# Kernel tuning notes

Hardware: AMD Instinct MI355X
Metric: run time of the kernel (lower is better)

## Reference

```python
import jax, jax.numpy as jnp
import numpy as np

NUM_CLASSES = 80
C_OUT = 81
SCORE_THR = 0.02
IOU_THR = 0.45
TOPK = 1000
IMG_MAX = 320.0
STRIDES = [16, 32, 64, 107, 160, 320]
MIN_SIZES = [48, 100, 150, 202, 253, 304]
MAX_SIZES = [100, 150, 202, 253, 304, 320]
FEAT = [20, 10, 5, 3, 2, 1]
MAX_RATIO = float(abs(np.log(0.016)))


def _base_anchors(level):
    base = float(MIN_SIZES[level])
    scales = np.array([1.0, np.sqrt(MAX_SIZES[level] / MIN_SIZES[level])])
    ratios = np.array([1.0, 0.5, 2.0, 1.0 / 3.0, 3.0])
    h_ratios = np.sqrt(ratios)
    w_ratios = 1.0 / h_ratios
    # scale_major=False: scales vary along rows
    ws = (base * scales[:, None] * w_ratios[None, :]).reshape(-1)
    hs = (base * scales[:, None] * h_ratios[None, :]).reshape(-1)
    c = STRIDES[level] / 2.0
    ba = np.stack([c - 0.5 * ws, c - 0.5 * hs, c + 0.5 * ws, c + 0.5 * hs], -1)
    return ba[[0, 5, 1, 2, 3, 4]]  # index_select reorder, 6 anchors/loc


def _priors(level):
    ba = _base_anchors(level)
    f, s = FEAT[level], STRIDES[level]
    sx = np.arange(f, dtype=np.float64) * s
    xx = np.tile(sx, f)
    yy = np.repeat(sx, f)
    shifts = np.stack([xx, yy, xx, yy], -1)  # [f*f,4]
    return (ba[None, :, :] + shifts[:, None, :]).reshape(-1, 4).astype(np.float32)


PRIORS = [jnp.asarray(_priors(i)) for i in range(6)]


def delta2bbox(priors, deltas):
    stds = jnp.array([0.1, 0.1, 0.2, 0.2], dtype=deltas.dtype)
    d = deltas * stds
    pxy = (priors[:, :2] + priors[:, 2:]) * 0.5
    pwh = priors[:, 2:] - priors[:, :2]
    dwh = jnp.clip(d[:, 2:], -MAX_RATIO, MAX_RATIO)
    gxy = pxy + pwh * d[:, :2]
    gwh = pwh * jnp.exp(dwh)
    boxes = jnp.concatenate([gxy - 0.5 * gwh, gxy + 0.5 * gwh], -1)
    return jnp.clip(boxes, 0.0, IMG_MAX)


def _nms_keep(boxes, valid, iou_thr):
    # greedy NMS over score-sorted boxes; returns bool keep mask
    K = boxes.shape[0]
    area = (boxes[:, 2] - boxes[:, 0]) * (boxes[:, 3] - boxes[:, 1])
    lt = jnp.maximum(boxes[:, None, :2], boxes[None, :, :2])
    rb = jnp.minimum(boxes[:, None, 2:], boxes[None, :, 2:])
    wh = jnp.clip(rb - lt, 0.0)
    inter = wh[..., 0] * wh[..., 1]
    iou = inter / (area[:, None] + area[None, :] - inter)
    ar = jnp.arange(K)

    def body(i, alive):
        sup = (iou[i] > iou_thr) & (ar > i) & alive[i]
        return alive & ~sup

    return jax.lax.fori_loop(0, K, body, valid)


def _single_image(cls_list, bb_list):
    boxes_l, scores_l, labels_l, valid_l = [], [], [], []
    for cls, bb, priors in zip(cls_list, bb_list, PRIORS):
        probs = jax.nn.softmax(cls.transpose(1, 2, 0).reshape(-1, C_OUT), axis=-1)[:, :NUM_CLASSES]
        flat = probs.reshape(-1)  # [N*80]
        k = min(TOPK, flat.shape[0])
        masked = jnp.where(flat > SCORE_THR, flat, -1.0)
        vals, idx = jax.lax.top_k(masked, k)
        valid = vals > SCORE_THR
        a_idx = idx // NUM_CLASSES
        lbl = idx % NUM_CLASSES
        deltas = bb.transpose(1, 2, 0).reshape(-1, 4)[a_idx]
        boxes = delta2bbox(priors[a_idx], deltas)
        boxes_l.append(boxes)
        scores_l.append(jnp.where(valid, vals, 0.0))
        labels_l.append(lbl)
        valid_l.append(valid)
    boxes = jnp.concatenate(boxes_l, 0)   # [K,4]
    scores = jnp.concatenate(scores_l, 0)
    labels = jnp.concatenate(labels_l, 0)
    valid = jnp.concatenate(valid_l, 0)

    # batched (class-aware) NMS via per-class coordinate offsets
    max_coord = boxes.max()
    offsets = labels.astype(boxes.dtype) * (max_coord + 1.0)
    boxes_nms = boxes + offsets[:, None]
    order = jnp.argsort(-jnp.where(valid, scores, -jnp.inf))
    boxes_s = boxes[order]
    scores_s = scores[order]
    labels_s = labels[order]
    valid_s = valid[order]
    keep = jax.lax.stop_gradient(
        _nms_keep(jax.lax.stop_gradient(boxes_nms[order]), valid_s, IOU_THR))
    dets = jnp.concatenate([boxes_s, scores_s[:, None]], -1) * keep[:, None].astype(boxes.dtype)
    return dets, labels_s, keep


def setup_inputs() -> dict:
    key = jax.random.key(0)
    ks = jax.random.split(key, 12)
    B = 4
    inp = {}
    for i, f in enumerate(FEAT):
        inp[f"cls{i}"] = jax.random.normal(ks[i], (B, 486, f, f), dtype=jnp.float32)
        inp[f"bb{i}"] = jax.random.normal(ks[6 + i], (B, 24, f, f), dtype=jnp.float32)
    return inp


def reference(cls0, cls1, cls2, cls3, cls4, cls5, bb0, bb1, bb2, bb3, bb4, bb5):
    def one(c0, c1, c2, c3, c4, c5, b0, b1, b2, b3, b4, b5):
        return _single_image([c0, c1, c2, c3, c4, c5], [b0, b1, b2, b3, b4, b5])
    dets, labels, keep = jax.vmap(one)(cls0, cls1, cls2, cls3, cls4, cls5,
                                       bb0, bb1, bb2, bb3, bb4, bb5)
    return dets, labels, keep
```

## Files before the change

kernel.cpp:

```cpp
#include <hip/hip_runtime.h>
#include <stdint.h>

#define NB 4
#define KTOT 5480
#define PER_IMG 258720
#define SCORE_THR 0.02f
#define IOU_THR 0.45f
#define REL_BASE 0x3CA3D70Bu
#define JCH 10
#define JSZ 548
#define ICH 11
#define NMSCAP 512
#define HBINS 256
#define HPART 42

__constant__ int cFEAT[6]    = {20,10,5,3,2,1};
__constant__ int cSTRIDE[6]  = {16,32,64,107,160,320};
__constant__ int cMIN[6]     = {48,100,150,202,253,304};
__constant__ int cMAX[6]     = {100,150,202,253,304,320};
__constant__ int cNFLAT[6]   = {192000,48000,12000,4320,1920,480};
__constant__ int cFLATOFF[6] = {0,192000,240000,252000,256320,258240};
__constant__ int cKSEL[6]    = {1000,1000,1000,1000,1000,480};
__constant__ int cKOFF[6]    = {0,1000,2000,3000,4000,5000};
__constant__ double cRATIO[6] = {1.0,1.0,0.5,2.0,1.0/3.0,3.0};
__constant__ int eTLEV[24] = {0,0,0,0,0,0,0,0,0,0,0,0,0,0,0,0, 1,1,1,1, 2,3,4,5};
__constant__ int eTCHK[24] = {0,1,2,3,4,5,6,7,8,9,10,11,12,13,14,15, 0,1,2,3, 0,0,0,0};
__constant__ int eNCH[6]   = {16,4,1,1,1,1};
__constant__ int hL0[6]    = {0,42,54,60,66,72};
__constant__ int hLN[6]    = {42,12,6,6,6,6};

__device__ __forceinline__ unsigned long long mk_key(unsigned kb, int lev, unsigned idx) {
  return ((unsigned long long)kb << 21) |
         (unsigned long long)(0x1FFFFFu ^ (((unsigned)lev << 18) | idx));
}

__device__ __forceinline__ unsigned long long shfl64(unsigned long long x, int src) {
  int lo = __shfl((int)(unsigned)(x & 0xffffffffull), src);
  int hi = __shfl((int)(unsigned)(x >> 32), src);
  return ((unsigned long long)(unsigned)hi << 32) | (unsigned)lo;
}

__global__ __launch_bounds__(256) void k_softmax(
    const float* __restrict__ c0, const float* __restrict__ c1,
    const float* __restrict__ c2, const float* __restrict__ c3,
    const float* __restrict__ c4, const float* __restrict__ c5,
    float* __restrict__ scores, unsigned* __restrict__ bhist,
    unsigned* __restrict__ obmax_u, unsigned* __restrict__ ctrl)
{
  int t = blockIdx.x;
  int tid = threadIdx.x;
  if (t == 0) {
    if (tid < 4) obmax_u[tid] = 0u;
    if (tid >= 64 && tid < 256) ctrl[tid - 64] = 0u;
  }
  int b = t / 78, rem = t % 78;
  int lev, a, cb;
  if (rem < 42)      { lev = 0; a = rem / 7;         cb = (rem % 7) * 64; }
  else if (rem < 54) { lev = 1; a = (rem - 42) >> 1; cb = ((rem - 42) & 1) * 64; }
  else               { lev = 2 + (rem - 54) / 6; a = (rem - 54) % 6; cb = 0; }
  const float* cls = (lev==0)?c0:(lev==1)?c1:(lev==2)?c2:(lev==3)?c3:(lev==4)?c4:c5;
  int f = cFEAT[lev], ff = f * f;
  int ncell = ff - cb; if (ncell > 64) ncell = 64;

  __shared__ float tile[81 * 64];
  __shared__ unsigned hcnt[HBINS];
  if (tid < HBINS) hcnt[tid] = 0;
  const float* base = cls + (size_t)(b * 486 + a * 81) * ff + cb;
  for (int t2 = tid; t2 < 81 * 64; t2 += 256) {
    int c = t2 >> 6, cell = t2 & 63;
    if (cell < ncell)
      tile[(c << 6) | (cell ^ (c & 63))] = base[c * ff + cell];
  }
  __syncthreads();

  int lane = tid & 63, w = tid >> 6;
  for (int cell = w; cell < ncell; cell += 4) {
    float v1 = tile[(lane << 6) | (cell ^ lane)];
    float v2 = (lane <= 16) ? tile[((lane + 64) << 6) | (cell ^ lane)]
                            : __uint_as_float(0xff800000u);
    float mx = fmaxf(v1, v2);
    #pragma unroll
    for (int m = 32; m; m >>= 1) mx = fmaxf(mx, __shfl_xor(mx, m));
    float e1 = expf(v1 - mx);
    float e2 = (lane <= 16) ? expf(v2 - mx) : 0.f;
    float sm = e1 + e2;
    #pragma unroll
    for (int m = 32; m; m >>= 1) sm += __shfl_xor(sm, m);
    int row = (cb + cell) * 6 + a;
    float* out = scores + (size_t)b * PER_IMG + cFLATOFF[lev] + row * 80;
    float p1 = e1 / sm;
    out[lane] = (p1 > SCORE_THR) ? p1 : -1.f;
    if (p1 > SCORE_THR)
      atomicAdd(&hcnt[(__float_as_uint(p1) - REL_BASE) >> 18], 1u);
    if (lane < 16) {
      float p2 = e2 / sm;
      out[lane + 64] = (p2 > SCORE_THR) ? p2 : -1.f;
      if (p2 > SCORE_THR)
        atomicAdd(&hcnt[(__float_as_uint(p2) - REL_BASE) >> 18], 1u);
    }
  }
  __syncthreads();
  int task = b * 6 + lev;
  int j = rem - hL0[lev];
  if (tid < HBINS)
    bhist[((size_t)task * HBINS + tid) * HPART + j] = hcnt[tid];
}

__global__ __launch_bounds__(256) void k_emit(
    const float* __restrict__ scores, const unsigned* __restrict__ bhist,
    unsigned* __restrict__ ctrl, unsigned long long* __restrict__ selkeys,
    unsigned long long* __restrict__ eqg)
{
  int b = blockIdx.x / 24, ent = blockIdx.x % 24;
  int lev = eTLEV[ent], chk = eTCHK[ent];
  int task = b * 6 + lev;
  int n = cNFLAT[lev];
  int tid = threadIdx.x;
  const float* s = scores + (size_t)b * PER_IMG + cFLATOFF[lev];
  unsigned long long* out = selkeys + (size_t)b * KTOT + cKOFF[lev];

  if (lev == 5) {
    for (int i = tid; i < n; i += 256) {
      float v = s[i];
      unsigned kb = (v > SCORE_THR) ? __float_as_uint(v) : 0u;
      out[i] = mk_key(kb, lev, (unsigned)i);
    }
    return;
  }

  unsigned k = (unsigned)cKSEL[lev];
  __shared__ unsigned long long wbuf[1024];
  __shared__ unsigned long long ebuf[4096];
  __shared__ unsigned sc[256];
  __shared__ unsigned wcnt, ecnt, sbw, sbe, sh_mode, sh_b1;

  {
    const unsigned* hb = bhist + ((size_t)task * HBINS + tid) * HPART;
    int np = hLN[lev];
    unsigned cnt = 0;
    for (int j = 0; j < np; ++j) cnt += hb[j];
    sc[tid] = cnt;
    __syncthreads();
    for (int off = 1; off < 256; off <<= 1) {
      unsigned cur = sc[tid];
      unsigned add = (tid + off < 256) ? sc[tid + off] : 0u;
      __syncthreads();
      sc[tid] = cur + add;
      __syncthreads();
    }
    unsigned c = sc[0];
    if (tid == 0 && c < k) sh_mode = 1u;
    if (c >= k) {
      unsigned above = (tid == 255) ? 0u : sc[tid + 1];
      if (above < k && above + cnt >= k) { sh_mode = 0u; sh_b1 = (unsigned)tid; }
    }
    if (tid == 0) { wcnt = 0; ecnt = 0; }
    __syncthreads();
  }
  unsigned mode = sh_mode;

  int csz = n / eNCH[lev];
  int start = chk * csz;
  const float4* s4 = (const float4*)(s + start);
  int n4 = csz >> 2;

  if (mode == 0u) {
    unsigned b1 = sh_b1;
    unsigned base_lo = REL_BASE + (b1 << 18);
    unsigned base_hi = base_lo + (1u << 18);
    #pragma unroll 4
    for (int i0 = tid; i0 < n4; i0 += 256) {
      float4 vv = s4[i0];
      #pragma unroll
      for (int e2 = 0; e2 < 4; ++e2) {
        float v = (e2==0)?vv.x:(e2==1)?vv.y:(e2==2)?vv.z:vv.w;
        if (v > SCORE_THR) {
          unsigned kb = __float_as_uint(v);
          unsigned idx = (unsigned)(start + i0 * 4 + e2);
          if (kb >= base_hi) {
            unsigned p = atomicAdd(&wcnt, 1u);
            if (p < 1024u) wbuf[p] = mk_key(kb, lev, idx);
          } else if (kb >= base_lo) {
            unsigned p = atomicAdd(&ecnt, 1u);
            if (p < 4096u) ebuf[p] = mk_key(kb, lev, idx);
          }
        }
      }
    }
  } else {
    #pragma unroll 4
    for (int i0 = tid; i0 < n4; i0 += 256) {
      float4 vv = s4[i0];
      #pragma unroll
      for (int e2 = 0; e2 < 4; ++e2) {
        float v = (e2==0)?vv.x:(e2==1)?vv.y:(e2==2)?vv.z:vv.w;
        if (v > SCORE_THR) {
          unsigned p = atomicAdd(&wcnt, 1u);
          if (p < 1024u) wbuf[p] = mk_key(__float_as_uint(v), lev,
                                          (unsigned)(start + i0 * 4 + e2));
        }
      }
    }
  }
  __syncthreads();
  if (tid == 0) {
    sbw = atomicAdd(&ctrl[task * 8 + 2], wcnt);
    sbe = atomicAdd(&ctrl[task * 8 + 3], ecnt);
  }
  __syncthreads();
  unsigned nw = (wcnt < 1024u) ? wcnt : 1024u;
  unsigned ne = (ecnt < 4096u) ? ecnt : 4096u;
  unsigned bw = sbw, be = sbe;
  for (unsigned t = tid; t < nw; t += 256) out[bw + t] = wbuf[t];
  for (unsigned t = tid; t < ne; t += 256) {
    unsigned g = be + t;
    if (g < 4096u) eqg[(size_t)task * 4096 + g] = ebuf[t];
  }
}

__global__ __launch_bounds__(1024) void k_finalize(
    const float* __restrict__ scores, const unsigned* __restrict__ bhist,
    const unsigned* __restrict__ ctrl, unsigned long long* __restrict__ selkeys,
    const unsigned long long* __restrict__ eqg)
{
  int task = blockIdx.x;
  int b = task / 6, lev = task % 6;
  if (lev == 5) return;
  int tid = threadIdx.x;
  unsigned k = (unsigned)cKSEL[lev];
  int n = cNFLAT[lev];
  const float* s = scores + (size_t)b * PER_IMG + cFLATOFF[lev];
  unsigned long long* out = selkeys + (size_t)b * KTOT + cKOFF[lev];
  unsigned levtag = (unsigned)lev << 18;

  __shared__ unsigned long long eqb[4096];
  __shared__ unsigned sc[1024];
  __shared__ unsigned sh_cnt, sh_eq, sh_byte, sh_r;

  unsigned hval = 0;
  if (tid < HBINS) {
    const unsigned* hb = bhist + ((size_t)task * HBINS + tid) * HPART;
    int np = hLN[lev];
    for (int j = 0; j < np; ++j) hval += hb[j];
  }
  sc[tid] = (tid < HBINS) ? hval : 0u;
  __syncthreads();
  for (int off = 128; off >= 1; off >>= 1) {
    if (tid < off) sc[tid] += sc[tid + off];
    __syncthreads();
  }
  unsigned c = sc[0];
  __syncthreads();
  unsigned mode = (c >= k) ? 0u : 1u;
  bool done = false;

  if (mode == 0u) {
    unsigned cnt = ctrl[task * 8 + 2];
    unsigned e = ctrl[task * 8 + 3];
    unsigned need = k - cnt;
    if (e <= 4096u) {
      const unsigned long long* eq = eqg + (size_t)task * 4096;
      if (e == need) {
        for (unsigned t = tid; t < need; t += 1024) out[cnt + t] = eq[t];
      } else {
        unsigned P = 1; while (P < e) P <<= 1;
        for (unsigned t = tid; t < P; t += 1024) eqb[t] = (t < e) ? eq[t] : 0ull;
        __syncthreads();
        for (unsigned sz = 2; sz <= P; sz <<= 1)
          for (unsigned st = sz >> 1; st; st >>= 1) {
            for (unsigned w = tid; w < P / 2; w += 1024) {
              unsigned i = ((w & ~(st - 1)) << 1) | (w & (st - 1));
              unsigned l = i | st;
              bool up = ((i & sz) == 0);
              unsigned long long A = eqb[i], B = eqb[l];
              if ((A < B) == up) { eqb[i] = B; eqb[l] = A; }
            }
            __syncthreads();
          }
        for (unsigned t = tid; t < need; t += 1024) out[cnt + t] = eqb[t];
      }
      done = true;
    }
  } else {
    unsigned c2 = ctrl[task * 8 + 2];
    unsigned need = k - c2;
    unsigned base = 0;
    for (int start = 0; start < n && base < need; start += 1024) {
      int i = start + tid;
      unsigned pred = (i < n && !(s[i] > SCORE_THR)) ? 1u : 0u;
      sc[tid] = pred;
      __syncthreads();
      for (int off = 1; off < 1024; off <<= 1) {
        unsigned add = (tid >= off) ? sc[tid - off] : 0u;
        unsigned v = sc[tid];
        __syncthreads();
        sc[tid] = v + add;
        __syncthreads();
      }
      unsigned incl = sc[tid];
      unsigned total = sc[1023];
      unsigned excl = incl - pred;
      if (pred && (base + excl) < need)
        out[c2 + base + excl] =
            (unsigned long long)(0x1FFFFFu ^ (levtag | (unsigned)i));
      __syncthreads();
      base += total;
    }
    done = true;
  }

  if (!done) {
    unsigned* hist = sc;
    unsigned* equ = (unsigned*)eqb;
    unsigned prefix = 0, r = k;
    for (int pass = 3; pass >= 0; --pass) {
      int shift = pass * 8;
      for (int i = tid; i < 256; i += 1024) hist[i] = 0;
      __syncthreads();
      for (int i = tid; i < n; i += 1024) {
        float v = s[i];
        unsigned kb = (v > SCORE_THR) ? __float_as_uint(v) : 0u;
        bool match = (pass == 3) || (((kb ^ prefix) >> (shift + 8)) == 0u);
        if (match) atomicAdd(&hist[(kb >> shift) & 255u], 1u);
      }
      __syncthreads();
      if (tid == 0) {
        unsigned cum = 0, byte = 0, rr = r;
        for (int bb = 255; bb >= 0; --bb) {
          unsigned hh = hist[bb];
          if (cum + hh >= r) { byte = (unsigned)bb; rr = r - cum; break; }
          cum += hh;
        }
        sh_byte = byte; sh_r = rr;
      }
      __syncthreads();
      prefix |= (sh_byte << shift);
      r = sh_r;
      __syncthreads();
    }
    unsigned Kstar = prefix;
    if (tid == 0) { sh_cnt = 0; sh_eq = 0; }
    __syncthreads();
    for (int i = tid; i < n; i += 1024) {
      float v = s[i];
      unsigned kb = (v > SCORE_THR) ? __float_as_uint(v) : 0u;
      if (kb > Kstar) {
        unsigned slot = atomicAdd(&sh_cnt, 1u);
        out[slot] = mk_key(kb, lev, (unsigned)i);
      } else if (kb == Kstar) {
        unsigned es = atomicAdd(&sh_eq, 1u);
        if (es < 4096u) equ[es] = (unsigned)i;
      }
    }
    __syncthreads();
    unsigned m = sh_cnt;
    unsigned e2 = (sh_eq < 4096u) ? sh_eq : 4096u;
    unsigned need2 = k - m;
    if (e2 > need2) {
      unsigned P = 1; while (P < e2) P <<= 1;
      for (unsigned t = tid; t < P; t += 1024) if (t >= e2) equ[t] = 0xFFFFFFFFu;
      __syncthreads();
      for (unsigned sz = 2; sz <= P; sz <<= 1)
        for (unsigned st = sz >> 1; st; st >>= 1) {
          for (unsigned w = tid; w < P / 2; w += 1024) {
            unsigned i = ((w & ~(st - 1)) << 1) | (w & (st - 1));
            unsigned l = i | st;
            bool up = ((i & sz) == 0);
            unsigned A = equ[i], B = equ[l];
            if ((A > B) == up) { equ[i] = B; equ[l] = A; }
          }
          __syncthreads();
        }
    }
    __syncthreads();
    for (unsigned t = tid; t < need2; t += 1024)
      out[m + t] = ((unsigned long long)Kstar << 21) |
                   (unsigned long long)(0x1FFFFFu ^ (levtag | equ[t]));
  }
}

__global__ __launch_bounds__(512) void k_rank(
    const unsigned long long* __restrict__ selkeys, unsigned* __restrict__ rank_part)
{
  int blk = blockIdx.x;
  int jc = blk % JCH;
  int rest = blk / JCH;
  int ic = rest % ICH, b = rest / ICH;
  int tid = threadIdx.x;
  __shared__ __align__(16) unsigned long long sk[JSZ];
  const unsigned long long* keys = selkeys + (size_t)b * KTOT;
  for (int j = tid; j < JSZ; j += 512) sk[j] = keys[jc * JSZ + j];
  int i = ic * 512 + tid;
  unsigned long long mk = (i < KTOT) ? keys[i] : 0ull;
  __syncthreads();
  unsigned r = 0;
  const ulonglong2* sk2 = (const ulonglong2*)sk;
  #pragma unroll 8
  for (int j = 0; j < JSZ / 2; ++j) {
    ulonglong2 kk = sk2[j];
    r += (kk.x > mk) ? 1u : 0u;
    r += (kk.y > mk) ? 1u : 0u;
  }
  if (i < KTOT) rank_part[((size_t)jc * NB + b) * KTOT + i] = r;
}

__global__ __launch_bounds__(512) void k_decode(
    const unsigned long long* __restrict__ selkeys, const unsigned* __restrict__ rank_part,
    const float* __restrict__ g0, const float* __restrict__ g1,
    const float* __restrict__ g2, const float* __restrict__ g3,
    const float* __restrict__ g4, const float* __restrict__ g5,
    float* __restrict__ boxes, float* __restrict__ oscore,
    unsigned char* __restrict__ lab8, unsigned* __restrict__ obmax_u,
    float* __restrict__ outp)
{
  int b = blockIdx.x / ICH, ic = blockIdx.x % ICH;
  int tid = threadIdx.x;
  int i = ic * 512 + tid;
  __shared__ double ba[6][6][4];
  if (tid < 36) {
    int lev = tid / 6, a = tid % 6;
    double base = (double)cMIN[lev];
    double scl = (a == 1) ? sqrt((double)cMAX[lev] / (double)cMIN[lev]) : 1.0;
    double hr = sqrt(cRATIO[a]);
    double wr = 1.0 / hr;
    double wsz = base * scl * wr;
    double hsz = base * scl * hr;
    double cc = (double)cSTRIDE[lev] / 2.0;
    ba[lev][a][0] = cc - 0.5 * wsz;
    ba[lev][a][1] = cc - 0.5 * hsz;
    ba[lev][a][2] = cc + 0.5 * wsz;
    ba[lev][a][3] = cc + 0.5 * hsz;
  }
  __syncthreads();

  float lmax = 0.f;
  if (i < KTOT) {
    unsigned long long mk = selkeys[(size_t)b * KTOT + i];
    unsigned r = 0;
    #pragma unroll
    for (int jc = 0; jc < JCH; ++jc)
      r += rank_part[((size_t)jc * NB + b) * KTOT + i];
    unsigned tag = 0x1FFFFFu ^ (unsigned)(mk & 0x1FFFFFull);
    int lev = tag >> 18;
    int fi = tag & 0x3FFFF;
    unsigned vb2 = (unsigned)(mk >> 21);
    int valid = (vb2 != 0u);
    float score = valid ? __uint_as_float(vb2) : 0.f;
    int label = fi % 80;
    int arow = fi / 80;
    int a = arow % 6, cell = arow / 6;
    int f = cFEAT[lev], ff = f * f;
    int x = cell % f, y = cell / f;
    const float* gb = (lev==0)?g0:(lev==1)?g1:(lev==2)?g2:(lev==3)?g3:(lev==4)?g4:g5;
    const float* pb = gb + (size_t)(b * 24 + a * 4) * ff + y * f + x;
    float d0 = pb[0] * 0.1f, d1 = pb[ff] * 0.1f;
    float d2 = pb[2 * ff] * 0.2f, d3 = pb[3 * ff] * 0.2f;
    const float MR = (float)4.135166556742356;
    d2 = fminf(fmaxf(d2, -MR), MR);
    d3 = fminf(fmaxf(d3, -MR), MR);
    double shx = (double)(x * cSTRIDE[lev]);
    double shy = (double)(y * cSTRIDE[lev]);
    float p0 = (float)(ba[lev][a][0] + shx);
    float p1 = (float)(ba[lev][a][1] + shy);
    float p2 = (float)(ba[lev][a][2] + shx);
    float p3 = (float)(ba[lev][a][3] + shy);
    float pxc = (p0 + p2) * 0.5f, pyc = (p1 + p3) * 0.5f;
    float pw = p2 - p0, ph = p3 - p1;
    float gx = pxc + pw * d0, gy = pyc + ph * d1;
    float gw = pw * expf(d2), gh = ph * expf(d3);
    float x1 = gx - 0.5f * gw, y1 = gy - 0.5f * gh;
    float x2 = gx + 0.5f * gw, y2 = gy + 0.5f * gh;
    x1 = fminf(fmaxf(x1, 0.f), 320.f);
    y1 = fminf(fmaxf(y1, 0.f), 320.f);
    x2 = fminf(fmaxf(x2, 0.f), 320.f);
    y2 = fminf(fmaxf(y2, 0.f), 320.f);
    size_t o = (size_t)b * KTOT + (size_t)r;
    boxes[o * 4 + 0] = x1; boxes[o * 4 + 1] = y1;
    boxes[o * 4 + 2] = x2; boxes[o * 4 + 3] = y2;
    oscore[o] = score;
    lab8[o] = valid ? (unsigned char)label : (unsigned char)0xFF;
    outp[(size_t)NB * KTOT * 5 + o] = (float)label;
    if (!valid) {
      float* det = outp + o * 5;
      det[0] = 0.f; det[1] = 0.f; det[2] = 0.f; det[3] = 0.f; det[4] = 0.f;
      outp[(size_t)NB * KTOT * 6 + o] = 0.f;
    }
    lmax = fmaxf(fmaxf(x1, y1), fmaxf(x2, y2));
  }
  #pragma unroll
  for (int m = 32; m; m >>= 1) lmax = fmaxf(lmax, __shfl_xor(lmax, m));
  if ((tid & 63) == 0) atomicMax(&obmax_u[b], __float_as_uint(lmax));
}

__global__ __launch_bounds__(256) void k_nms(
    const float* __restrict__ boxes, const float* __restrict__ oscore,
    const unsigned char* __restrict__ lab8, const unsigned* __restrict__ obmax_u,
    float* __restrict__ out)
{
  int blk = blockIdx.x;
  int b = blk / 80, cls = blk % 80;
  int tid = threadIdx.x;
  int lane = tid & 63, w = tid >> 6;

  __shared__ unsigned short list[NMSCAP];
  __shared__ float ox1[NMSCAP], oy1[NMSCAP], ox2[NMSCAP], oy2[NMSCAP];
  __shared__ float oar[NMSCAP], osc[NMSCAP];
  __shared__ float rx1[NMSCAP], ry1[NMSCAP], rx2[NMSCAP], ry2[NMSCAP];
  __shared__ unsigned long long mask[NMSCAP][8];
  __shared__ unsigned ccnt[24], cbase[24];
  __shared__ int sh_n;
  __shared__ unsigned long long alive_s[8];

  float ofs = (float)cls * (__uint_as_float(obmax_u[b]) + 1.0f);
  const unsigned* lb32 = (const unsigned*)(lab8 + (size_t)b * KTOT);

  unsigned long long balA[6][4];
  #pragma unroll
  for (int ci = 0; ci < 6; ++ci) {
    int chunk = w + ci * 4;
    unsigned v = 0xFFFFFFFFu;
    if (chunk < 22) {
      int u = chunk * 64 + lane;
      if (u < KTOT / 4) v = lb32[u];
    }
    unsigned long long m0 = __ballot(((v      ) & 0xFFu) == (unsigned)cls);
    unsigned long long m1 = __ballot(((v >>  8) & 0xFFu) == (unsigned)cls);
    unsigned long long m2 = __ballot(((v >> 16) & 0xFFu) == (unsigned)cls);
    unsigned long long m3 = __ballot(((v >> 24) & 0xFFu) == (unsigned)cls);
    balA[ci][0] = m0; balA[ci][1] = m1; balA[ci][2] = m2; balA[ci][3] = m3;
    if (chunk < 22 && lane == 0)
      ccnt[chunk] = (unsigned)(__popcll(m0) + __popcll(m1) + __popcll(m2) + __popcll(m3));
  }
  __syncthreads();
  if (tid == 0) {
    unsigned tot = 0;
    for (int c = 0; c < 22; ++c) { cbase[c] = tot; tot += ccnt[c]; }
    sh_n = (tot < NMSCAP) ? (int)tot : NMSCAP;
  }
  __syncthreads();
  int n = sh_n;
  unsigned long long blt = (lane == 0) ? 0ull : ((~0ull) >> (64 - lane));
  #pragma unroll
  for (int ci = 0; ci < 6; ++ci) {
    int chunk = w + ci * 4;
    if (chunk < 22) {
      unsigned pos = cbase[chunk];
      unsigned below = (unsigned)(__popcll(balA[ci][0] & blt) + __popcll(balA[ci][1] & blt) +
                                  __popcll(balA[ci][2] & blt) + __popcll(balA[ci][3] & blt));
      unsigned within = 0;
      #pragma unroll
      for (int k = 0; k < 4; ++k) {
        if ((balA[ci][k] >> lane) & 1ull) {
          unsigned mypos = pos + below + within;
          if (mypos < NMSCAP) list[mypos] = (unsigned short)(chunk * 256 + lane * 4 + k);
          ++within;
        }
      }
    }
  }
  __syncthreads();

  for (int t = tid; t < n; t += 256) {
    int pos = list[t];
    size_t o = (size_t)b * KTOT + pos;
    float4 bb = *(const float4*)(boxes + o * 4);
    rx1[t] = bb.x; ry1[t] = bb.y; rx2[t] = bb.z; ry2[t] = bb.w;
    float a1 = bb.x + ofs, b1 = bb.y + ofs, a2 = bb.z + ofs, b2 = bb.w + ofs;
    ox1[t] = a1; oy1[t] = b1; ox2[t] = a2; oy2[t] = b2;
    oar[t] = (a2 - a1) * (b2 - b1);
    osc[t] = oscore[o];
  }
  __syncthreads();

  int nw = (n + 63) >> 6;
  for (int i = tid; i < n; i += 256) {
    float ax1 = ox1[i], ay1 = oy1[i], ax2 = ox2[i], ay2 = oy2[i], aar = oar[i];
    int w0 = i >> 6;
    for (int wd = w0; wd < nw; ++wd) {
      unsigned long long m = 0;
      int jbase = wd << 6;
      int jend = n - jbase; if (jend > 64) jend = 64;
      for (int jj = 0; jj < jend; ++jj) {
        int j = jbase + jj;
        if (j > i) {
          float ix1 = fmaxf(ax1, ox1[j]);
          float iy1 = fmaxf(ay1, oy1[j]);
          float ix2 = fminf(ax2, ox2[j]);
          float iy2 = fminf(ay2, oy2[j]);
          float iw = fmaxf(ix2 - ix1, 0.f);
          float ih = fmaxf(iy2 - iy1, 0.f);
          float inter = iw * ih;
          float iou = inter / (aar + oar[j] - inter);
          if (iou > IOU_THR) m |= (1ull << jj);
        }
      }
      mask[i][wd] = m;
    }
  }
  __syncthreads();

  if (w == 0) {
    unsigned long long aw = 0;
    if (lane < nw) {
      int rem = n - (lane << 6);
      aw = (rem >= 64) ? ~0ull : ((1ull << rem) - 1ull);
    }
    for (int i = 0; i < n; ++i) {
      int wi = i >> 6;
      unsigned long long mrow = (lane >= wi && lane < nw) ? mask[i][lane] : 0ull;
      unsigned long long tw = shfl64(aw, wi);
      if ((tw >> (i & 63)) & 1ull) aw &= ~mrow;
    }
    if (lane < 8) alive_s[lane] = aw;
  }
  __syncthreads();

  for (int t = tid; t < n; t += 256) {
    float kf = ((alive_s[t >> 6] >> (t & 63)) & 1ull) ? 1.f : 0.f;
    int pos = list[t];
    size_t o = (size_t)b * KTOT + pos;
    float* det = out + o * 5;
    det[0] = rx1[t] * kf; det[1] = ry1[t] * kf;
    det[2] = rx2[t] * kf; det[3] = ry2[t] * kf;
    det[4] = osc[t] * kf;
    out[(size_t)NB * KTOT * 6 + o] = kf;
  }
}

extern "C" void kernel_launch(void* const* d_in, const int* in_sizes, int n_in,
                              void* d_out, int out_size, void* d_ws, size_t ws_size,
                              hipStream_t stream) {
  (void)in_sizes; (void)n_in; (void)out_size; (void)ws_size;
  const float* cls[6]; const float* bbx[6];
  for (int i = 0; i < 6; ++i) {
    cls[i] = (const float*)d_in[2 * i];
    bbx[i] = (const float*)d_in[2 * i + 1];
  }
  char* ws = (char*)d_ws;
  float* scores = (float*)ws;
  unsigned* rank_part = (unsigned*)ws;
  unsigned long long* selkeys = (unsigned long long*)(ws + 4139520);
  float* boxes  = (float*)(ws + 4314880);
  float* oscore = (float*)(ws + 4665600);
  unsigned char* lab8 = (unsigned char*)(ws + 4753280);
  unsigned* obmax_u = (unsigned*)(ws + 5016320);
  unsigned* ctrl    = (unsigned*)(ws + 5016576);
  unsigned* bhist   = (unsigned*)(ws + 5017600);
  unsigned long long* eqg = (unsigned long long*)(ws + 6049792);

  k_softmax<<<NB * 78, 256, 0, stream>>>(cls[0], cls[1], cls[2], cls[3], cls[4], cls[5],
                                         scores, bhist, obmax_u, ctrl);
  k_emit<<<NB * 24, 256, 0, stream>>>(scores, bhist, ctrl, selkeys, eqg);
  k_finalize<<<24, 1024, 0, stream>>>(scores, bhist, ctrl, selkeys, eqg);
  k_rank<<<NB * ICH * JCH, 512, 0, stream>>>(selkeys, rank_part);
  k_decode<<<NB * ICH, 512, 0, stream>>>(selkeys, rank_part, bbx[0], bbx[1], bbx[2],
                                         bbx[3], bbx[4], bbx[5], boxes, oscore, lab8,
                                         obmax_u, (float*)d_out);
  k_nms<<<NB * 80, 256, 0, stream>>>(boxes, oscore, lab8, obmax_u, (float*)d_out);
}
```

Measured before the change: 96.12 us.

## Fuse rank computation into decode kernel and drop rank partial buffer

Merges the separate rank kernel into the decode kernel: each thread now counts how many selected keys exceed its own by scanning all keys of its image directly from global memory. This removes one kernel launch and the rank_part write/read round trip. In exchange each thread does the full O(K) comparison serially with far fewer blocks, so parallelism drops and per-thread latency grows.

```diff
diff --git a/kernel.cpp b/kernel.cpp
--- a/kernel.cpp
+++ b/kernel.cpp
@@ -7,9 +7,7 @@
 #define SCORE_THR 0.02f
 #define IOU_THR 0.45f
 #define REL_BASE 0x3CA3D70Bu
-#define JCH 10
-#define JSZ 548
-#define ICH 11
+#define ICH2 22
 #define NMSCAP 512
 #define HBINS 256
 #define HPART 42
@@ -379,33 +377,8 @@
   }
 }
 
-__global__ __launch_bounds__(512) void k_rank(
-    const unsigned long long* __restrict__ selkeys, unsigned* __restrict__ rank_part)
-{
-  int blk = blockIdx.x;
-  int jc = blk % JCH;
-  int rest = blk / JCH;
-  int ic = rest % ICH, b = rest / ICH;
-  int tid = threadIdx.x;
-  __shared__ __align__(16) unsigned long long sk[JSZ];
-  const unsigned long long* keys = selkeys + (size_t)b * KTOT;
-  for (int j = tid; j < JSZ; j += 512) sk[j] = keys[jc * JSZ + j];
-  int i = ic * 512 + tid;
-  unsigned long long mk = (i < KTOT) ? keys[i] : 0ull;
-  __syncthreads();
-  unsigned r = 0;
-  const ulonglong2* sk2 = (const ulonglong2*)sk;
-  #pragma unroll 8
-  for (int j = 0; j < JSZ / 2; ++j) {
-    ulonglong2 kk = sk2[j];
-    r += (kk.x > mk) ? 1u : 0u;
-    r += (kk.y > mk) ? 1u : 0u;
-  }
-  if (i < KTOT) rank_part[((size_t)jc * NB + b) * KTOT + i] = r;
-}
-
-__global__ __launch_bounds__(512) void k_decode(
-    const unsigned long long* __restrict__ selkeys, const unsigned* __restrict__ rank_part,
+__global__ __launch_bounds__(256) void k_rankdec(
+    const unsigned long long* __restrict__ selkeys,
     const float* __restrict__ g0, const float* __restrict__ g1,
     const float* __restrict__ g2, const float* __restrict__ g3,
     const float* __restrict__ g4, const float* __restrict__ g5,
@@ -413,9 +386,9 @@
     unsigned char* __restrict__ lab8, unsigned* __restrict__ obmax_u,
     float* __restrict__ outp)
 {
-  int b = blockIdx.x / ICH, ic = blockIdx.x % ICH;
+  int b = blockIdx.x / ICH2, ic = blockIdx.x % ICH2;
   int tid = threadIdx.x;
-  int i = ic * 512 + tid;
+  int i = ic * 256 + tid;
   __shared__ double ba[6][6][4];
   if (tid < 36) {
     int lev = tid / 6, a = tid % 6;
@@ -431,15 +404,23 @@
     ba[lev][a][2] = cc + 0.5 * wsz;
     ba[lev][a][3] = cc + 0.5 * hsz;
   }
+
+  const unsigned long long* keys = selkeys + (size_t)b * KTOT;
+  unsigned long long mk = (i < KTOT) ? keys[i] : 0ull;
+  unsigned r = 0;
+  {
+    const ulonglong2* k2 = (const ulonglong2*)keys;
+    #pragma unroll 8
+    for (int j = 0; j < KTOT / 2; ++j) {
+      ulonglong2 kk = k2[j];
+      r += (kk.x > mk) ? 1u : 0u;
+      r += (kk.y > mk) ? 1u : 0u;
+    }
+  }
   __syncthreads();
 
   float lmax = 0.f;
   if (i < KTOT) {
-    unsigned long long mk = selkeys[(size_t)b * KTOT + i];
-    unsigned r = 0;
-    #pragma unroll
-    for (int jc = 0; jc < JCH; ++jc)
-      r += rank_part[((size_t)jc * NB + b) * KTOT + i];
     unsigned tag = 0x1FFFFFu ^ (unsigned)(mk & 0x1FFFFFull);
     int lev = tag >> 18;
     int fi = tag & 0x3FFFF;
@@ -638,7 +619,6 @@
   }
   char* ws = (char*)d_ws;
   float* scores = (float*)ws;
-  unsigned* rank_part = (unsigned*)ws;
   unsigned long long* selkeys = (unsigned long long*)(ws + 4139520);
   float* boxes  = (float*)(ws + 4314880);
   float* oscore = (float*)(ws + 4665600);
@@ -652,9 +632,8 @@
                                          scores, bhist, obmax_u, ctrl);
   k_emit<<<NB * 24, 256, 0, stream>>>(scores, bhist, ctrl, selkeys, eqg);
   k_finalize<<<24, 1024, 0, stream>>>(scores, bhist, ctrl, selkeys, eqg);
-  k_rank<<<NB * ICH * JCH, 512, 0, stream>>>(selkeys, rank_part);
-  k_decode<<<NB * ICH, 512, 0, stream>>>(selkeys, rank_part, bbx[0], bbx[1], bbx[2],
-                                         bbx[3], bbx[4], bbx[5], boxes, oscore, lab8,
-                                         obmax_u, (float*)d_out);
+  k_rankdec<<<NB * ICH2, 256, 0, stream>>>(selkeys, bbx[0], bbx[1], bbx[2], bbx[3],
+                                           bbx[4], bbx[5], boxes, oscore, lab8,
+                                           obmax_u, (float*)d_out);
   k_nms<<<NB * 80, 256, 0, stream>>>(boxes, oscore, lab8, obmax_u, (float*)d_out);
 }
```

Result: slower. 267.5 us (+178.3%).
